# Performance work log

Measured on AMD Instinct MI355X. Metric: run time of the kernel, lower is better.

## Reference

```python
import jax, jax.numpy as jnp
import numpy as np

N = 200000      # nodes
E = 6400000     # edges (avg degree 32)
F_IN = 4        # node feature dim used by GraphConv
H = 184         # 4 * scale(46)
MD_H = 16       # min_distance MLP width
L1 = 188        # H + 4
A = 5           # action_space


def _uniform(k, shape, fan_in):
    b = 1.0 / np.sqrt(fan_in)
    return jax.random.uniform(k, shape, jnp.float32, -b, b)


def setup_inputs() -> dict:
    key = jax.random.key(0)
    ks = jax.random.split(key, 16)
    node_feat = jax.random.normal(ks[0], (N, 6), jnp.float32)
    edge_index = jax.random.randint(ks[1], (2, E), 0, N, dtype=jnp.int32)
    edge_weight = jax.random.uniform(ks[2], (E,), jnp.float32)
    center_idx = 0
    return {
        "node_feat": node_feat,
        "edge_index": edge_index,
        "edge_weight": edge_weight,
        "center_idx": center_idx,
        # GraphConv(4, 184): lin_rel (with bias) applied to aggregated msgs, lin_root (no bias) to x
        "W_rel": _uniform(ks[3], (F_IN, H), F_IN),
        "b_rel": _uniform(ks[4], (H,), F_IN),
        "W_root": _uniform(ks[5], (F_IN, H), F_IN),
        # linear2: 2 -> 16
        "W2": _uniform(ks[6], (2, MD_H), 2),
        "b2": _uniform(ks[7], (MD_H,), 2),
        # linear2_1: 16 -> 16
        "W21": _uniform(ks[8], (MD_H, MD_H), MD_H),
        "b21": _uniform(ks[9], (MD_H,), MD_H),
        # linear1: 200 -> 188
        "W1": _uniform(ks[10], (H + MD_H, L1), H + MD_H),
        "b1": _uniform(ks[11], (L1,), H + MD_H),
        # linear4: 188 -> 5
        "W4": _uniform(ks[12], (L1, A), L1),
        "b4": _uniform(ks[13], (A,), L1),
    }


def reference(node_feat, edge_index, edge_weight, center_idx,
              W_rel, b_rel, W_root, W2, b2, W21, b21, W1, b1, W4, b4):
    x = node_feat[:, :4]                                   # [N, 4]
    src, dst = edge_index[0], edge_index[1]
    # GraphConv message: e_ji * x_j, mean-aggregated at target nodes
    msg = x[src] * edge_weight[:, None]                    # [E, 4]
    agg = jax.ops.segment_sum(msg, dst, num_segments=N)    # [N, 4]
    deg = jax.ops.segment_sum(jnp.ones((E,), jnp.float32), dst, num_segments=N)
    mean = agg / jnp.maximum(deg, 1.0)[:, None]
    h = jax.nn.relu(mean @ W_rel + b_rel + x @ W_root)     # [N, 184]
    # global_max_pool with batch=None -> max over all nodes
    x1 = jnp.max(h, axis=0, keepdims=True)                 # [1, 184]
    x2 = h[center_idx:center_idx + 1]                      # [1, 184]
    g = x2 - x1
    md = node_feat[center_idx, 4:].reshape(1, 2)           # [1, 2]
    md = jax.nn.relu(md @ W2 + b2)
    md = jax.nn.relu(md @ W21 + b21)
    g = jnp.concatenate([g, md], axis=1)                   # [1, 200]
    g = jax.nn.relu(g @ W1 + b1)
    return g @ W4 + b4                                     # [1, 5]
```

## Files before the change

### kernel.cpp

```cpp
#include <hip/hip_runtime.h>

#define H 184
#define MDH 16
#define L1D 188
#define BBITS 9
#define BSZ 512
#define KMAX 512
#define CHUNKE 4096
#define SSUB 4
#define SREC_CAP 4416
#define RPT 18

__global__ void zero_kernel(int* __restrict__ p, int n) {
    int i = blockIdx.x * blockDim.x + threadIdx.x;
    if (i < n) p[i] = 0;
}

__global__ __launch_bounds__(256) void pack_kernel(
        const float* __restrict__ nf, float4* __restrict__ x4,
        int* __restrict__ zp, int zn, int N) {
    __shared__ float s[256 * 6];
    int base = blockIdx.x * 256;
    int t = threadIdx.x;
    if (blockIdx.x == 0 && zp != nullptr)
        for (int i = t; i < zn; i += 256) zp[i] = 0;
    for (int i = t; i < 256 * 6; i += 256) {
        int gi = base * 6 + i;
        s[i] = (gi < N * 6) ? nf[gi] : 0.0f;
    }
    __syncthreads();
    int n = base + t;
    if (n < N)
        x4[n] = make_float4(s[t * 6], s[t * 6 + 1], s[t * 6 + 2], s[t * 6 + 3]);
}

__device__ __forceinline__ void scan512(const int* __restrict__ cnt,
                                        int* __restrict__ sc,
                                        int* __restrict__ wtot, int t) {
    int wv = t >> 6, ln = t & 63;
    int base = wv * 128 + 2 * ln;
    int a = cnt[base], b = cnt[base + 1];
    int s0 = a + b;
    int x = s0;
    #pragma unroll
    for (int d = 1; d < 64; d <<= 1) {
        int y = __shfl_up(x, d, 64);
        if (ln >= d) x += y;
    }
    if (ln == 63) wtot[wv] = x;
    __syncthreads();
    int woff = 0;
    #pragma unroll
    for (int wq = 0; wq < 3; ++wq) woff += (wq < wv) ? wtot[wq] : 0;
    int excl = woff + x - s0;
    sc[base]     = excl + a;
    sc[base + 1] = excl + s0;
    __syncthreads();
}

__global__ __launch_bounds__(256) void partition_cs_kernel(
        const int* __restrict__ ei, const float* __restrict__ ew,
        int* __restrict__ cursor, uint2* __restrict__ region,
        int E, int K, int CAP) {
    __shared__ uint2 srec[CHUNKE];
    __shared__ int cnt[KMAX];
    __shared__ int sc[KMAX];
    __shared__ int wbase[KMAX];
    __shared__ int wtot[4];
    int t = threadIdx.x;
    int c = blockIdx.x;

    int e0 = c * CHUNKE;
    int e1 = min(E, e0 + CHUNKE);

    cnt[t] = 0;
    cnt[t + 256] = 0;
    __syncthreads();

    unsigned meta[16];
    unsigned srcv[16];
    unsigned wv[16];
    #pragma unroll
    for (int j = 0; j < 4; ++j) {
        int e = e0 + t * 4 + j * 1024;
        int4 d4 = make_int4(0, 0, 0, 0);
        int4 s4 = make_int4(0, 0, 0, 0);
        float4 w4 = make_float4(0.f, 0.f, 0.f, 0.f);
        bool full = (e + 3 < e1);
        if (full) {
            d4 = *(const int4*)(ei + E + e);
            s4 = *(const int4*)(ei + e);
            w4 = *(const float4*)(ew + e);
        }
        #pragma unroll
        for (int q = 0; q < 4; ++q) {
            int idx = j * 4 + q;
            meta[idx] = 0xFFFFFFFFu;
            int eq = e + q;
            if (eq < e1) {
                int dst = full ? (q == 0 ? d4.x : q == 1 ? d4.y : q == 2 ? d4.z : d4.w)
                               : ei[E + eq];
                int src = full ? (q == 0 ? s4.x : q == 1 ? s4.y : q == 2 ? s4.z : s4.w)
                               : ei[eq];
                float w = full ? (q == 0 ? w4.x : q == 1 ? w4.y : q == 2 ? w4.z : w4.w)
                               : ew[eq];
                int k = ((unsigned)dst) >> BBITS;
                int r = atomicAdd(&cnt[k], 1);
                meta[idx] = ((unsigned)k << 21) | ((unsigned)r << 9)
                          | ((unsigned)dst & (BSZ - 1));
                srcv[idx] = (unsigned)src;
                wv[idx]   = __float_as_uint(w);
            }
        }
    }
    __syncthreads();

    scan512(cnt, sc, wtot, t);

    #pragma unroll
    for (int kq = 0; kq < 2; ++kq) {
        int k = t + kq * 256;
        int ck = cnt[k];
        int pos = sc[k] - ck;
        int b = 0;
        if (k < K && ck > 0) {
            b = atomicAdd(&cursor[k], ck);
            if (b + ck > CAP) b = CAP - ck;
        }
        wbase[k] = b;
        cnt[k] = pos;
    }
    __syncthreads();

    #pragma unroll
    for (int j = 0; j < 16; ++j) {
        if (meta[j] != 0xFFFFFFFFu) {
            int k  = meta[j] >> 21;
            int r  = (meta[j] >> 9) & 0xFFF;
            int dl = meta[j] & (BSZ - 1);
            int slot = cnt[k] + r;
            srec[slot] = make_uint2(((unsigned)dl << 18) | srcv[j], wv[j]);
        }
    }
    __syncthreads();

    #pragma unroll
    for (int kq = 0; kq < 2; ++kq) {
        int k = t + kq * 256;
        int pos = cnt[k];
        int ck = sc[k] - pos;
        if (k < K && ck > 0) {
            uint2* dstp = region + (size_t)k * CAP + wbase[k];
            for (int i = 0; i < ck; ++i)
                dstp[i] = srec[pos + i];
        }
    }
}

__global__ __launch_bounds__(256) void bucket_sort_accum_kernel(
        const float4* __restrict__ x4, const uint2* __restrict__ region,
        const int* __restrict__ cursor, float* __restrict__ partials, int CAP) {
    __shared__ uint2 srec[SREC_CAP];
    __shared__ int cnt[BSZ], sc[BSZ];
    __shared__ int wtot[4];
    int k = blockIdx.x / SSUB;
    int s = blockIdx.x % SSUB;
    int t = threadIdx.x;

    for (int i = t; i < BSZ; i += 256) cnt[i] = 0;
    __syncthreads();

    int len = cursor[k];
    if (len > CAP) len = CAP;
    const uint2* base = region + (size_t)k * CAP;
    int i0 = (int)(((long long)len * s) / SSUB);
    int i1 = (int)(((long long)len * (s + 1)) / SSUB);

    uint2 rec[RPT];
    unsigned rb[RPT];
    #pragma unroll
    for (int j = 0; j < RPT; ++j) {
        int i = i0 + t + j * 256;
        rb[j] = 0xFFFFFFFFu;
        if (i < i1) {
            uint2 r = base[i];
            int bin = r.x >> 18;
            int rk = atomicAdd(&cnt[bin], 1);
            rec[j] = r;
            rb[j] = ((unsigned)bin << 13) | (unsigned)rk;
        }
    }
    __syncthreads();

    scan512(cnt, sc, wtot, t);

    #pragma unroll
    for (int j = 0; j < RPT; ++j) {
        if (rb[j] != 0xFFFFFFFFu) {
            int bin = rb[j] >> 13;
            int rk  = rb[j] & 0x1FFF;
            int slot = sc[bin] - cnt[bin] + rk;
            srec[slot] = rec[j];
        }
    }
    __syncthreads();

    int dA = t, dB = t + 256;
    int cA = cnt[dA], startA = sc[dA] - cA;
    int cB = cnt[dB], startB = sc[dB] - cB;
    float4 aA = make_float4(0.f, 0.f, 0.f, 0.f);
    float4 aB = make_float4(0.f, 0.f, 0.f, 0.f);
    int m = max(cA, cB);
    for (int i = 0; i < m; ++i) {
        if (i < cA) {
            uint2 r = srec[startA + i];
            float4 xv = x4[r.x & 0x3FFFFu];
            float w = __uint_as_float(r.y);
            aA.x += xv.x * w; aA.y += xv.y * w;
            aA.z += xv.z * w; aA.w += xv.w * w;
        }
        if (i < cB) {
            uint2 r = srec[startB + i];
            float4 xv = x4[r.x & 0x3FFFFu];
            float w = __uint_as_float(r.y);
            aB.x += xv.x * w; aB.y += xv.y * w;
            aB.z += xv.z * w; aB.w += xv.w * w;
        }
    }
    float* pp = partials + (size_t)blockIdx.x * (BSZ * 5);
    pp[0 * BSZ + dA] = aA.x;
    pp[1 * BSZ + dA] = aA.y;
    pp[2 * BSZ + dA] = aA.z;
    pp[3 * BSZ + dA] = aA.w;
    pp[4 * BSZ + dA] = (float)cA;
    pp[0 * BSZ + dB] = aB.x;
    pp[1 * BSZ + dB] = aB.y;
    pp[2 * BSZ + dB] = aB.z;
    pp[3 * BSZ + dB] = aB.w;
    pp[4 * BSZ + dB] = (float)cB;
}

__global__ __launch_bounds__(256) void bucket_reduce_kernel(
        const float* __restrict__ partials, float* __restrict__ agg,
        float* __restrict__ deg, int N) {
    __shared__ float acc[BSZ * 5];
    int k = blockIdx.x;
    int t = threadIdx.x;
    const float* b = partials + (size_t)k * SSUB * (BSZ * 5);
    for (int j = t; j < BSZ * 5; j += 256) {
        float v = 0.0f;
        for (int s = 0; s < SSUB; ++s) v += b[(size_t)s * (BSZ * 5) + j];
        acc[j] = v;
    }
    __syncthreads();
    for (int d = t; d < BSZ; d += 256) {
        int n = (k << BBITS) + d;
        if (n < N) {
            ((float4*)agg)[n] = make_float4(acc[0 * BSZ + d], acc[1 * BSZ + d],
                                            acc[2 * BSZ + d], acc[3 * BSZ + d]);
            deg[n] = acc[4 * BSZ + d];
        }
    }
}

__global__ __launch_bounds__(256) void edge_atomic_kernel(
        const float* __restrict__ nf, const int* __restrict__ ei,
        const float* __restrict__ ew, float* __restrict__ agg,
        float* __restrict__ deg, int E) {
    int e = blockIdx.x * blockDim.x + threadIdx.x;
    if (e >= E) return;
    int src = ei[e];
    int dst = ei[E + e];
    float w = ew[e];
    const float2* xr = (const float2*)(nf + (size_t)src * 6);
    float2 x01 = xr[0];
    float2 x23 = xr[1];
    float* a = agg + (size_t)dst * 4;
    atomicAdd(a + 0, x01.x * w);
    atomicAdd(a + 1, x01.y * w);
    atomicAdd(a + 2, x23.x * w);
    atomicAdd(a + 3, x23.y * w);
    atomicAdd(deg + dst, 1.0f);
}

__global__ __launch_bounds__(192) void node_kernel(
        const float4* __restrict__ x4,
        const float* __restrict__ agg,
        const float* __restrict__ deg,
        const float* __restrict__ W_rel, const float* __restrict__ b_rel,
        const float* __restrict__ W_root,
        const int*   __restrict__ centerp,
        unsigned int* __restrict__ xmax_bits,
        float* __restrict__ h0,
        int N, int nodes_per_block) {
    int j = threadIdx.x;
    if (j >= H) return;
    int center = *centerp;
    int n0 = blockIdx.x * nodes_per_block;
    int n1 = n0 + nodes_per_block;
    if (n1 > N) n1 = N;

    float wr0 = W_rel[0 * H + j], wr1 = W_rel[1 * H + j];
    float wr2 = W_rel[2 * H + j], wr3 = W_rel[3 * H + j];
    float wo0 = W_root[0 * H + j], wo1 = W_root[1 * H + j];
    float wo2 = W_root[2 * H + j], wo3 = W_root[3 * H + j];
    float b = b_rel[j];

    float mx = 0.0f;
    for (int n = n0; n < n1; ++n) {
        float4 a = ((const float4*)agg)[n];
        float inv = 1.0f / fmaxf(deg[n], 1.0f);
        float4 x = x4[n];
        float v = b
                + (a.x * inv) * wr0 + (a.y * inv) * wr1
                + (a.z * inv) * wr2 + (a.w * inv) * wr3
                + x.x * wo0 + x.y * wo1 + x.z * wo2 + x.w * wo3;
        v = fmaxf(v, 0.0f);
        mx = fmaxf(mx, v);
        if (n == center) h0[j] = v;
    }
    atomicMax(xmax_bits + j, __float_as_uint(mx));
}

__global__ __launch_bounds__(256) void final_kernel(
        const float* __restrict__ nf,
        const int*   __restrict__ centerp,
        const unsigned int* __restrict__ xmax_bits,
        const float* __restrict__ h0,
        const float* __restrict__ W2,  const float* __restrict__ b2,
        const float* __restrict__ W21, const float* __restrict__ b21,
        const float* __restrict__ W1,  const float* __restrict__ b1,
        const float* __restrict__ W4,  const float* __restrict__ b4,
        float* __restrict__ out) {
    __shared__ float gin[H + MDH];
    __shared__ float md0[MDH];
    __shared__ float g1[L1D];
    int t = threadIdx.x;
    int center = *centerp;

    if (t < H) gin[t] = h0[t] - __uint_as_float(xmax_bits[t]);
    if (t < MDH) {
        float m0 = nf[(size_t)center * 6 + 4];
        float m1 = nf[(size_t)center * 6 + 5];
        md0[t] = fmaxf(m0 * W2[t] + m1 * W2[MDH + t] + b2[t], 0.0f);
    }
    __syncthreads();
    if (t < MDH) {
        float s = b21[t];
        for (int k = 0; k < MDH; ++k) s += md0[k] * W21[k * MDH + t];
        gin[H + t] = fmaxf(s, 0.0f);
    }
    __syncthreads();
    if (t < L1D) {
        float s = b1[t];
        for (int k = 0; k < H + MDH; ++k) s += gin[k] * W1[k * L1D + t];
        g1[t] = fmaxf(s, 0.0f);
    }
    __syncthreads();
    if (t < 5) {
        float s = b4[t];
        for (int k = 0; k < L1D; ++k) s += g1[k] * W4[k * 5 + t];
        out[t] = s;
    }
}

extern "C" void kernel_launch(void* const* d_in, const int* in_sizes, int n_in,
                              void* d_out, int out_size, void* d_ws, size_t ws_size,
                              hipStream_t stream) {
    const float* nf      = (const float*)d_in[0];
    const int*   ei      = (const int*)  d_in[1];
    const float* ew      = (const float*)d_in[2];
    const int*   centerp = (const int*)  d_in[3];
    const float* W_rel   = (const float*)d_in[4];
    const float* b_rel   = (const float*)d_in[5];
    const float* W_root  = (const float*)d_in[6];
    const float* W2      = (const float*)d_in[7];
    const float* b2      = (const float*)d_in[8];
    const float* W21     = (const float*)d_in[9];
    const float* b21     = (const float*)d_in[10];
    const float* W1      = (const float*)d_in[11];
    const float* b1      = (const float*)d_in[12];
    const float* W4      = (const float*)d_in[13];
    const float* b4      = (const float*)d_in[14];
    float* out = (float*)d_out;

    const int N = in_sizes[0] / 6;
    const int E = in_sizes[1] / 2;
    const int K = (N + BSZ - 1) >> BBITS;
    const int nchunks = (E + CHUNKE - 1) / CHUNKE;
    int cap = E / K + E / K / 16 + 256;
    cap = (cap + 63) & ~63;

    int*          cursor   = (int*)d_ws;
    unsigned int* xmax     = (unsigned int*)(cursor + 512);
    float*        h0       = (float*)(xmax + H);
    float*        agg      = h0 + H;
    float*        deg      = agg + (size_t)N * 4;
    float4*       x4       = (float4*)(deg + N);
    float*        partials = (float*)(x4 + N);
    uint2*        region   = (uint2*)(partials + (size_t)K * SSUB * (BSZ * 5));

    size_t need = (size_t)((char*)(region + (size_t)K * cap) - (char*)d_ws);
    bool fast = (ws_size >= need) && (K <= KMAX) && (N <= (1 << 18))
             && ((E & 3) == 0)
             && ((cap + SSUB - 1) / SSUB <= SREC_CAP);

    if (fast) {
        pack_kernel<<<(N + 255) / 256, 256, 0, stream>>>(nf, x4, cursor, 512 + H, N);
        partition_cs_kernel<<<nchunks, 256, 0, stream>>>(ei, ew, cursor, region,
                                                         E, K, cap);
        bucket_sort_accum_kernel<<<K * SSUB, 256, 0, stream>>>(x4, region, cursor,
                                                               partials, cap);
        bucket_reduce_kernel<<<K, 256, 0, stream>>>(partials, agg, deg, N);

        const int blocks = 2048;
        const int npb = (N + blocks - 1) / blocks;
        node_kernel<<<blocks, 192, 0, stream>>>(x4, agg, deg, W_rel, b_rel, W_root,
                                                centerp, xmax, h0, N, npb);
    } else {
        zero_kernel<<<(N * 5 + 255) / 256, 256, 0, stream>>>((int*)agg, N * 5);
        zero_kernel<<<1, 256, 0, stream>>>((int*)xmax, H);
        pack_kernel<<<(N + 255) / 256, 256, 0, stream>>>(nf, x4, nullptr, 0, N);
        edge_atomic_kernel<<<(E + 255) / 256, 256, 0, stream>>>(nf, ei, ew, agg, deg, E);
        const int blocks = 2048;
        const int npb = (N + blocks - 1) / blocks;
        node_kernel<<<blocks, 192, 0, stream>>>(x4, agg, deg, W_rel, b_rel, W_root,
                                                centerp, xmax, h0, N, npb);
    }

    final_kernel<<<1, 256, 0, stream>>>(nf, centerp, xmax, h0,
                                        W2, b2, W21, b21, W1, b1, W4, b4, out);
}
```

Measured before the change: 333.3 us.

## Fuse bucket reduce and final MLP into predecessors via last-block tickets

Removes the separate bucket_reduce and final kernel launches. The last of the SSUB sub-blocks for each bucket, chosen by an atomic done-counter, sums the partials, and the last node_kernel block, chosen by a global ticket, runs the small MLP head. This saves two kernel launches and their inter-kernel gaps. In exchange it adds threadfences and atomics to every block and leaves the final reduction running on only a few blocks.

After: 655.8 us. 96.8% more time.

```diff
diff --git a/kernel.cpp b/kernel.cpp
--- a/kernel.cpp
+++ b/kernel.cpp
@@ -159,10 +159,13 @@
 
 __global__ __launch_bounds__(256) void bucket_sort_accum_kernel(
         const float4* __restrict__ x4, const uint2* __restrict__ region,
-        const int* __restrict__ cursor, float* __restrict__ partials, int CAP) {
+        const int* __restrict__ cursor, float* __restrict__ partials,
+        int* __restrict__ done, float* __restrict__ agg,
+        float* __restrict__ deg, int CAP, int N) {
     __shared__ uint2 srec[SREC_CAP];
     __shared__ int cnt[BSZ], sc[BSZ];
     __shared__ int wtot[4];
+    __shared__ int lastf;
     int k = blockIdx.x / SSUB;
     int s = blockIdx.x % SSUB;
     int t = threadIdx.x;
@@ -238,27 +241,29 @@
     pp[2 * BSZ + dB] = aB.z;
     pp[3 * BSZ + dB] = aB.w;
     pp[4 * BSZ + dB] = (float)cB;
-}
-
-__global__ __launch_bounds__(256) void bucket_reduce_kernel(
-        const float* __restrict__ partials, float* __restrict__ agg,
-        float* __restrict__ deg, int N) {
-    __shared__ float acc[BSZ * 5];
-    int k = blockIdx.x;
-    int t = threadIdx.x;
+
+    __threadfence();
+    __syncthreads();
+    if (t == 0) lastf = (atomicAdd(&done[k], 1) == SSUB - 1) ? 1 : 0;
+    __syncthreads();
+    if (!lastf) return;
+    __threadfence();
+
+    float* facc = (float*)srec;
     const float* b = partials + (size_t)k * SSUB * (BSZ * 5);
     for (int j = t; j < BSZ * 5; j += 256) {
         float v = 0.0f;
-        for (int s = 0; s < SSUB; ++s) v += b[(size_t)s * (BSZ * 5) + j];
-        acc[j] = v;
+        #pragma unroll
+        for (int s2 = 0; s2 < SSUB; ++s2) v += b[(size_t)s2 * (BSZ * 5) + j];
+        facc[j] = v;
     }
     __syncthreads();
     for (int d = t; d < BSZ; d += 256) {
         int n = (k << BBITS) + d;
         if (n < N) {
-            ((float4*)agg)[n] = make_float4(acc[0 * BSZ + d], acc[1 * BSZ + d],
-                                            acc[2 * BSZ + d], acc[3 * BSZ + d]);
-            deg[n] = acc[4 * BSZ + d];
+            ((float4*)agg)[n] = make_float4(facc[0 * BSZ + d], facc[1 * BSZ + d],
+                                            facc[2 * BSZ + d], facc[3 * BSZ + d]);
+            deg[n] = facc[4 * BSZ + d];
         }
     }
 }
@@ -292,51 +297,56 @@
         const int*   __restrict__ centerp,
         unsigned int* __restrict__ xmax_bits,
         float* __restrict__ h0,
-        int N, int nodes_per_block) {
-    int j = threadIdx.x;
-    if (j >= H) return;
-    int center = *centerp;
-    int n0 = blockIdx.x * nodes_per_block;
-    int n1 = n0 + nodes_per_block;
-    if (n1 > N) n1 = N;
-
-    float wr0 = W_rel[0 * H + j], wr1 = W_rel[1 * H + j];
-    float wr2 = W_rel[2 * H + j], wr3 = W_rel[3 * H + j];
-    float wo0 = W_root[0 * H + j], wo1 = W_root[1 * H + j];
-    float wo2 = W_root[2 * H + j], wo3 = W_root[3 * H + j];
-    float b = b_rel[j];
-
-    float mx = 0.0f;
-    for (int n = n0; n < n1; ++n) {
-        float4 a = ((const float4*)agg)[n];
-        float inv = 1.0f / fmaxf(deg[n], 1.0f);
-        float4 x = x4[n];
-        float v = b
-                + (a.x * inv) * wr0 + (a.y * inv) * wr1
-                + (a.z * inv) * wr2 + (a.w * inv) * wr3
-                + x.x * wo0 + x.y * wo1 + x.z * wo2 + x.w * wo3;
-        v = fmaxf(v, 0.0f);
-        mx = fmaxf(mx, v);
-        if (n == center) h0[j] = v;
-    }
-    atomicMax(xmax_bits + j, __float_as_uint(mx));
-}
-
-__global__ __launch_bounds__(256) void final_kernel(
+        int N, int nodes_per_block, int nblocks,
+        int* __restrict__ ticket,
         const float* __restrict__ nf,
-        const int*   __restrict__ centerp,
-        const unsigned int* __restrict__ xmax_bits,
-        const float* __restrict__ h0,
         const float* __restrict__ W2,  const float* __restrict__ b2,
         const float* __restrict__ W21, const float* __restrict__ b21,
         const float* __restrict__ W1,  const float* __restrict__ b1,
         const float* __restrict__ W4,  const float* __restrict__ b4,
         float* __restrict__ out) {
+    __shared__ int lastf;
+    int j = threadIdx.x;
+    int center = *centerp;
+
+    if (j < H) {
+        int n0 = blockIdx.x * nodes_per_block;
+        int n1 = n0 + nodes_per_block;
+        if (n1 > N) n1 = N;
+
+        float wr0 = W_rel[0 * H + j], wr1 = W_rel[1 * H + j];
+        float wr2 = W_rel[2 * H + j], wr3 = W_rel[3 * H + j];
+        float wo0 = W_root[0 * H + j], wo1 = W_root[1 * H + j];
+        float wo2 = W_root[2 * H + j], wo3 = W_root[3 * H + j];
+        float b = b_rel[j];
+
+        float mx = 0.0f;
+        for (int n = n0; n < n1; ++n) {
+            float4 a = ((const float4*)agg)[n];
+            float inv = 1.0f / fmaxf(deg[n], 1.0f);
+            float4 x = x4[n];
+            float v = b
+                    + (a.x * inv) * wr0 + (a.y * inv) * wr1
+                    + (a.z * inv) * wr2 + (a.w * inv) * wr3
+                    + x.x * wo0 + x.y * wo1 + x.z * wo2 + x.w * wo3;
+            v = fmaxf(v, 0.0f);
+            mx = fmaxf(mx, v);
+            if (n == center) h0[j] = v;
+        }
+        atomicMax(xmax_bits + j, __float_as_uint(mx));
+    }
+
+    __threadfence();
+    __syncthreads();
+    if (j == 0) lastf = (atomicAdd(ticket, 1) == nblocks - 1) ? 1 : 0;
+    __syncthreads();
+    if (!lastf) return;
+    __threadfence();
+
     __shared__ float gin[H + MDH];
     __shared__ float md0[MDH];
     __shared__ float g1[L1D];
-    int t = threadIdx.x;
-    int center = *centerp;
+    int t = j;
 
     if (t < H) gin[t] = h0[t] - __uint_as_float(xmax_bits[t]);
     if (t < MDH) {
@@ -347,19 +357,19 @@
     __syncthreads();
     if (t < MDH) {
         float s = b21[t];
-        for (int k = 0; k < MDH; ++k) s += md0[k] * W21[k * MDH + t];
+        for (int kk = 0; kk < MDH; ++kk) s += md0[kk] * W21[kk * MDH + t];
         gin[H + t] = fmaxf(s, 0.0f);
     }
     __syncthreads();
     if (t < L1D) {
         float s = b1[t];
-        for (int k = 0; k < H + MDH; ++k) s += gin[k] * W1[k * L1D + t];
+        for (int kk = 0; kk < H + MDH; ++kk) s += gin[kk] * W1[kk * L1D + t];
         g1[t] = fmaxf(s, 0.0f);
     }
     __syncthreads();
     if (t < 5) {
         float s = b4[t];
-        for (int k = 0; k < L1D; ++k) s += g1[k] * W4[k * 5 + t];
+        for (int kk = 0; kk < L1D; ++kk) s += g1[kk] * W4[kk * 5 + t];
         out[t] = s;
     }
 }
@@ -393,41 +403,40 @@
 
     int*          cursor   = (int*)d_ws;
     unsigned int* xmax     = (unsigned int*)(cursor + 512);
-    float*        h0       = (float*)(xmax + H);
+    int*          doneacc  = (int*)(xmax + H);
+    int*          ticket   = doneacc + 512;
+    float*        h0       = (float*)(ticket + 4);
     float*        agg      = h0 + H;
     float*        deg      = agg + (size_t)N * 4;
     float4*       x4       = (float4*)(deg + N);
     float*        partials = (float*)(x4 + N);
     uint2*        region   = (uint2*)(partials + (size_t)K * SSUB * (BSZ * 5));
+    const int ZN = 512 + H + 512 + 4;
 
     size_t need = (size_t)((char*)(region + (size_t)K * cap) - (char*)d_ws);
     bool fast = (ws_size >= need) && (K <= KMAX) && (N <= (1 << 18))
              && ((E & 3) == 0)
              && ((cap + SSUB - 1) / SSUB <= SREC_CAP);
 
+    const int blocks = 2048;
+    const int npb = (N + blocks - 1) / blocks;
+
     if (fast) {
-        pack_kernel<<<(N + 255) / 256, 256, 0, stream>>>(nf, x4, cursor, 512 + H, N);
+        pack_kernel<<<(N + 255) / 256, 256, 0, stream>>>(nf, x4, cursor, ZN, N);
         partition_cs_kernel<<<nchunks, 256, 0, stream>>>(ei, ew, cursor, region,
                                                          E, K, cap);
-        bucket_sort_accum_kernel<<<K * SSUB, 256, 0, stream>>>(x4, region, cursor,
-                                                               partials, cap);
-        bucket_reduce_kernel<<<K, 256, 0, stream>>>(partials, agg, deg, N);
-
-        const int blocks = 2048;
-        const int npb = (N + blocks - 1) / blocks;
-        node_kernel<<<blocks, 192, 0, stream>>>(x4, agg, deg, W_rel, b_rel, W_root,
-                                                centerp, xmax, h0, N, npb);
+        bucket_sort_accum_kernel<<<K * SSUB, 256, 0, stream>>>(
+            x4, region, cursor, partials, doneacc, agg, deg, cap, N);
+        node_kernel<<<blocks, 192, 0, stream>>>(
+            x4, agg, deg, W_rel, b_rel, W_root, centerp, xmax, h0,
+            N, npb, blocks, ticket, nf, W2, b2, W21, b21, W1, b1, W4, b4, out);
     } else {
         zero_kernel<<<(N * 5 + 255) / 256, 256, 0, stream>>>((int*)agg, N * 5);
-        zero_kernel<<<1, 256, 0, stream>>>((int*)xmax, H);
+        zero_kernel<<<1, 256, 0, stream>>>(cursor, ZN);
         pack_kernel<<<(N + 255) / 256, 256, 0, stream>>>(nf, x4, nullptr, 0, N);
         edge_atomic_kernel<<<(E + 255) / 256, 256, 0, stream>>>(nf, ei, ew, agg, deg, E);
-        const int blocks = 2048;
-        const int npb = (N + blocks - 1) / blocks;
-        node_kernel<<<blocks, 192, 0, stream>>>(x4, agg, deg, W_rel, b_rel, W_root,
-                                                centerp, xmax, h0, N, npb);
-    }
-
-    final_kernel<<<1, 256, 0, stream>>>(nf, centerp, xmax, h0,
-                                        W2, b2, W21, b21, W1, b1, W4, b4, out);
-}
+        node_kernel<<<blocks, 192, 0, stream>>>(
+            x4, agg, deg, W_rel, b_rel, W_root, centerp, xmax, h0,
+            N, npb, blocks, ticket, nf, W2, b2, W21, b21, W1, b1, W4, b4, out);
+    }
+}
```
